# Kernel optimization log

Measured on AMD Instinct MI355X. Metric: run time of the kernel, lower is better.

Reference implementation:

```python
import jax, jax.numpy as jnp
import numpy as np

DIM = 768
NUM_HEADS = 12
HEAD_DIM = DIM // NUM_HEADS
SCALE = HEAD_DIM ** -0.5


def setup_inputs() -> dict:
    key = jax.random.key(0)
    k1, k2, k3, k4, k5 = jax.random.split(key, 5)
    B, N, C = 4, 1024, DIM
    x = jax.random.normal(k1, (B, N, C), dtype=jnp.float32)
    # padding mask: last quarter of tokens masked out for half the batch
    mask = jnp.ones((B, N), dtype=bool)
    mask = mask.at[B // 2:, 3 * N // 4:].set(False)
    w_qkv = jax.random.normal(k2, (3 * C, C), dtype=jnp.float32) * (C ** -0.5)
    w_proj = jax.random.normal(k3, (C, C), dtype=jnp.float32) * (C ** -0.5)
    b_proj = jax.random.normal(k4, (C,), dtype=jnp.float32) * 0.02
    return {"x": x, "mask": mask, "w_qkv": w_qkv, "w_proj": w_proj, "b_proj": b_proj}


def reference(x, mask, w_qkv, w_proj, b_proj):
    B, N, C = x.shape
    H, D = NUM_HEADS, HEAD_DIM
    # qkv: Linear without bias -> [B, N, 3C] -> [3, B, H, N, D]
    qkv = jnp.einsum('bnc,oc->bno', x, w_qkv).reshape(B, N, 3, H, D)
    qkv = jnp.transpose(qkv, (2, 0, 3, 1, 4))
    q, k, v = qkv[0], qkv[1], qkv[2]
    attn = jnp.einsum('bhnd,bhmd->bhnm', q, k) * SCALE  # [B,H,N,N]
    # outer-product padding mask: mask[:,None,:] * mask[:,:,None], broadcast over heads
    pair_mask = (mask[:, None, :] & mask[:, :, None])[:, None, :, :]  # [B,1,N,N]
    mask_value = -jnp.finfo(attn.dtype).max
    attn = jnp.where(pair_mask, attn, mask_value)
    attn = jax.nn.softmax(attn, axis=-1)
    out = jnp.einsum('bhnm,bhmd->bhnd', attn, v)  # [B,H,N,D]
    out = jnp.transpose(out, (0, 2, 1, 3)).reshape(B, N, C)
    out = jnp.einsum('bnc,oc->bno', out, w_proj) + b_proj
    return out
```

## Files before the change

kernel.cpp:

```cpp
#include <hip/hip_runtime.h>
#include <hip/hip_fp16.h>
#include <float.h>

typedef _Float16 f16;
typedef __attribute__((ext_vector_type(4))) _Float16 f16x4;
typedef __attribute__((ext_vector_type(8))) _Float16 f16x8;
typedef __attribute__((ext_vector_type(4))) float f32x4;

#define NB 4
#define SEQ 1024
#define DIM 768
#define NH 12
#define HD 64
#define SCALE_F 0.125f
#define LOG2E 1.44269504088896f
#define NBH (NB * NH)

__device__ __forceinline__ void gload16(const f16* g, f16* lds) {
    __builtin_amdgcn_global_load_lds(
        (const __attribute__((address_space(1))) void*)g,
        (__attribute__((address_space(3))) void*)lds, 16, 0, 0);
}

__global__ __launch_bounds__(256) void cvt_mask_kernel(
    const float* __restrict__ X, const float* __restrict__ W1,
    const float* __restrict__ W2, const void* __restrict__ mask_raw,
    f16* __restrict__ Xh, f16* __restrict__ W1h, f16* __restrict__ W2h,
    int* __restrict__ mnorm) {
    const int A4 = (NB * SEQ * DIM) / 4;
    const int B4 = (3 * DIM * DIM) / 4;
    const int C4 = (DIM * DIM) / 4;
    const int tid = threadIdx.x;
    if (blockIdx.x == (unsigned)(A4 + B4 + C4 + 255) / 256) {
        __shared__ int is_u8;
        if (tid == 0) is_u8 = 0;
        __syncthreads();
        const unsigned int* u32 = (const unsigned int*)mask_raw;
        int bad = 0;
        for (int i = tid; i < (NB * SEQ) / 4; i += 256)
            if (u32[i] > 1u) bad = 1;
        if (bad) atomicOr(&is_u8, 1);
        __syncthreads();
        const int u8mode = is_u8;
        const unsigned char* u8 = (const unsigned char*)mask_raw;
        const int* i32 = (const int*)mask_raw;
        for (int i = tid; i < NB * SEQ; i += 256)
            mnorm[i] = u8mode ? (u8[i] != 0) : (i32[i] != 0);
        return;
    }
    int i = blockIdx.x * 256 + tid;
    const float* s; f16* d; int j;
    if (i < A4)                { s = X;  d = Xh;  j = i; }
    else if (i < A4 + B4)      { s = W1; d = W1h; j = i - A4; }
    else if (i < A4 + B4 + C4) { s = W2; d = W2h; j = i - A4 - B4; }
    else return;
    float4 v = ((const float4*)s)[j];
    f16x4 h;
    h[0] = (f16)v.x; h[1] = (f16)v.y; h[2] = (f16)v.z; h[3] = (f16)v.w;
    *(f16x4*)(d + 4 * (size_t)j) = h;
}

__global__ __launch_bounds__(256) void qkv_gemm_f16(
    const f16* __restrict__ Xh, const f16* __restrict__ Wh,
    f16* __restrict__ Qh, f16* __restrict__ Kh, f16* __restrict__ Vth) {
    __shared__ __align__(16) f16 Ah[128 * 32];
    __shared__ __align__(16) f16 Bh[128 * 32];
    const int tid = threadIdx.x;
    const int l = tid & 63, w = tid >> 6;
    const int lo = l & 15, hi = l >> 4;
    const int wm = w >> 1, wn = w & 1;
    const int m0 = blockIdx.y * 128, o0 = blockIdx.x * 128;

    f32x4 acc[4][4];
#pragma unroll
    for (int i = 0; i < 4; ++i)
#pragma unroll
        for (int j = 0; j < 4; ++j) { f32x4 z = {0.f, 0.f, 0.f, 0.f}; acc[i][j] = z; }

    const int gr = l >> 2;
    const int gc = (l & 3) * 8;
    const f16* gA = Xh + (size_t)(m0 + w * 32 + gr) * DIM + gc;
    const f16* gB = Wh + (size_t)(o0 + w * 32 + gr) * DIM + gc;
    f16* lA = Ah + (w * 2) * 512;
    f16* lB = Bh + (w * 2) * 512;

    for (int k0 = 0; k0 < DIM; k0 += 32) {
        __syncthreads();
        gload16(gA + k0,            lA);
        gload16(gA + k0 + 16 * DIM, lA + 512);
        gload16(gB + k0,            lB);
        gload16(gB + k0 + 16 * DIM, lB + 512);
        __syncthreads();
        f16x8 af[4], bf[4];
#pragma unroll
        for (int i = 0; i < 4; ++i)
            af[i] = *(const f16x8*)&Ah[(wm * 64 + i * 16 + lo) * 32 + hi * 8];
#pragma unroll
        for (int j = 0; j < 4; ++j)
            bf[j] = *(const f16x8*)&Bh[(wn * 64 + j * 16 + lo) * 32 + hi * 8];
#pragma unroll
        for (int i = 0; i < 4; ++i)
#pragma unroll
            for (int j = 0; j < 4; ++j)
                acc[i][j] = __builtin_amdgcn_mfma_f32_16x16x32_f16(af[i], bf[j], acc[i][j], 0, 0, 0);
    }

    const int oo = o0 + wn * 64;
    const int s = oo / DIM;
    const int hh = (oo % DIM) / HD;
    const int b = m0 >> 10;
    const int nbase = (m0 & 1023) + wm * 64;
    if (s < 2) {
        f16* dst = (s == 0) ? Qh : Kh;
        const float qs = (s == 0) ? SCALE_F * LOG2E : 1.0f;
        f16* base = dst + ((size_t)(b * NH + hh)) * SEQ * HD;
#pragma unroll
        for (int i = 0; i < 4; ++i)
#pragma unroll
            for (int r = 0; r < 4; ++r) {
                const int n = nbase + i * 16 + hi * 4 + r;
#pragma unroll
                for (int j = 0; j < 4; ++j)
                    base[(size_t)n * HD + j * 16 + lo] = (f16)(acc[i][j][r] * qs);
            }
    } else {
        f16* base = Vth + ((size_t)(b * NH + hh)) * HD * SEQ;
#pragma unroll
        for (int i = 0; i < 4; ++i) {
            const int n4 = nbase + i * 16 + hi * 4;
#pragma unroll
            for (int j = 0; j < 4; ++j) {
                const int d = j * 16 + lo;
                f16x4 pv;
#pragma unroll
                for (int r = 0; r < 4; ++r) pv[r] = (f16)acc[i][j][r];
                *(f16x4*)(base + (size_t)d * SEQ + n4) = pv;
            }
        }
    }
}

__global__ __launch_bounds__(256) void attn_f16(
    const f16* __restrict__ Qh, const f16* __restrict__ Kh,
    const f16* __restrict__ Vth, const int* __restrict__ mnorm,
    f16* __restrict__ Oh) {
    const int bh = blockIdx.y, b = bh / NH, hh = bh % NH;
    const int q0 = blockIdx.x * 64;
    const int tid = threadIdx.x;
    const int l = tid & 63, w = tid >> 6;
    const int lo = l & 15, hi = l >> 4;

    __shared__ __align__(16) f16 Ks[64][64];
    __shared__ __align__(16) f16 Vs[64][64];
    __shared__ __align__(16) f16 Ps[4][16][64];
    __shared__ int mks[64];

    const f16* Qp = Qh + (size_t)bh * SEQ * HD;
    const f16* Kp = Kh + (size_t)bh * SEQ * HD;
    const f16* Vp = Vth + (size_t)bh * HD * SEQ;

    f16x8 qa[2];
#pragma unroll
    for (int kk = 0; kk < 2; ++kk)
        qa[kk] = *(const f16x8*)(Qp + (size_t)(q0 + w * 16 + lo) * HD + kk * 32 + hi * 8);
    const int mq = mnorm[b * SEQ + q0 + w * 16 + lo];

    float m_run = -FLT_MAX, l_run = 0.f;
    f32x4 oacc[4];
#pragma unroll
    for (int n = 0; n < 4; ++n) { f32x4 z = {0.f, 0.f, 0.f, 0.f}; oacc[n] = z; }

    const int sr = tid >> 2, sc = (tid & 3) * 16;
    const int swz = (sr & 7) * 8;
    const int s8 = (lo & 7) * 8;

    f16x8 kr0, kr1, vr0, vr1; int mkr;
    kr0 = *(const f16x8*)(Kp + (size_t)sr * HD + sc);
    kr1 = *(const f16x8*)(Kp + (size_t)sr * HD + sc + 8);
    vr0 = *(const f16x8*)(Vp + (size_t)sr * SEQ + sc);
    vr1 = *(const f16x8*)(Vp + (size_t)sr * SEQ + sc + 8);
    mkr = mnorm[b * SEQ + l];

    for (int t = 0; t < SEQ / 64; ++t) {
        __syncthreads();
        *(f16x8*)&Ks[sr][sc ^ swz]       = kr0;
        *(f16x8*)&Ks[sr][(sc + 8) ^ swz] = kr1;
        *(f16x8*)&Vs[sr][sc ^ swz]       = vr0;
        *(f16x8*)&Vs[sr][(sc + 8) ^ swz] = vr1;
        if (tid < 64) mks[tid] = mkr;
        __syncthreads();
        if (t < SEQ / 64 - 1) {
            const int kv1 = (t + 1) * 64;
            kr0 = *(const f16x8*)(Kp + (size_t)(kv1 + sr) * HD + sc);
            kr1 = *(const f16x8*)(Kp + (size_t)(kv1 + sr) * HD + sc + 8);
            vr0 = *(const f16x8*)(Vp + (size_t)sr * SEQ + kv1 + sc);
            vr1 = *(const f16x8*)(Vp + (size_t)sr * SEQ + kv1 + sc + 8);
            mkr = mnorm[b * SEQ + kv1 + l];
        }

        f32x4 sf[4];
#pragma unroll
        for (int f = 0; f < 4; ++f) { f32x4 z = {0.f, 0.f, 0.f, 0.f}; sf[f] = z; }
#pragma unroll
        for (int kk = 0; kk < 2; ++kk)
#pragma unroll
            for (int f = 0; f < 4; ++f) {
                f16x8 kf = *(const f16x8*)&Ks[f * 16 + lo][(kk * 32 + hi * 8) ^ s8];
                sf[f] = __builtin_amdgcn_mfma_f32_16x16x32_f16(kf, qa[kk], sf[f], 0, 0, 0);
            }
#pragma unroll
        for (int f = 0; f < 4; ++f) {
            int mv[4];
            *(int4*)mv = *(const int4*)&mks[f * 16 + hi * 4];
#pragma unroll
            for (int r = 0; r < 4; ++r)
                sf[f][r] = (mq && mv[r]) ? sf[f][r] : -FLT_MAX;
        }
        float pm = -FLT_MAX;
#pragma unroll
        for (int f = 0; f < 4; ++f)
            pm = fmaxf(pm, fmaxf(fmaxf(sf[f][0], sf[f][1]), fmaxf(sf[f][2], sf[f][3])));
        pm = fmaxf(pm, __shfl_xor(pm, 16));
        pm = fmaxf(pm, __shfl_xor(pm, 32));
        const float mn = fmaxf(m_run, pm);
        const float alpha = exp2f(m_run - mn);
        m_run = mn;
        float rs = 0.f;
#pragma unroll
        for (int f = 0; f < 4; ++f)
#pragma unroll
            for (int r = 0; r < 4; ++r) {
                float p = exp2f(sf[f][r] - mn);
                sf[f][r] = p;
                rs += p;
            }
        rs += __shfl_xor(rs, 16);
        rs += __shfl_xor(rs, 32);
        l_run = l_run * alpha + rs;

#pragma unroll
        for (int f = 0; f < 4; ++f) {
            f16x4 pv;
#pragma unroll
            for (int r = 0; r < 4; ++r) pv[r] = (f16)sf[f][r];
            *(f16x4*)&Ps[w][lo][(f * 16 + hi * 4) ^ s8] = pv;
        }
        if (!__all(alpha == 1.0f)) {
            float ar[4];
#pragma unroll
            for (int r = 0; r < 4; ++r) ar[r] = __shfl(alpha, hi * 4 + r);
#pragma unroll
            for (int n = 0; n < 4; ++n)
#pragma unroll
                for (int r = 0; r < 4; ++r) oacc[n][r] *= ar[r];
        }
#pragma unroll
        for (int kk = 0; kk < 2; ++kk) {
            f16x8 pa = *(const f16x8*)&Ps[w][lo][(kk * 32 + hi * 8) ^ s8];
#pragma unroll
            for (int n = 0; n < 4; ++n) {
                f16x8 vb = *(const f16x8*)&Vs[n * 16 + lo][(kk * 32 + hi * 8) ^ s8];
                oacc[n] = __builtin_amdgcn_mfma_f32_16x16x32_f16(pa, vb, oacc[n], 0, 0, 0);
            }
        }
    }

    float il[4];
#pragma unroll
    for (int r = 0; r < 4; ++r) il[r] = __shfl(l_run, hi * 4 + r);
    f16* Op = Oh + ((size_t)b * SEQ + q0 + w * 16) * DIM + hh * HD;
#pragma unroll
    for (int r = 0; r < 4; ++r) {
        const float inv = 1.f / il[r];
#pragma unroll
        for (int n = 0; n < 4; ++n)
            Op[(size_t)(hi * 4 + r) * DIM + n * 16 + lo] = (f16)(oacc[n][r] * inv);
    }
}

__global__ __launch_bounds__(256) void proj_gemm_f16(
    const f16* __restrict__ Oh, const f16* __restrict__ Wph,
    const float* __restrict__ bp, float* __restrict__ out) {
    __shared__ __align__(16) f16 Ah[128 * 32];
    __shared__ __align__(16) f16 Bh[128 * 32];
    const int tid = threadIdx.x;
    const int l = tid & 63, w = tid >> 6;
    const int lo = l & 15, hi = l >> 4;
    const int wm = w >> 1, wn = w & 1;
    const int m0 = blockIdx.y * 128, o0 = blockIdx.x * 128;

    f32x4 acc[4][4];
#pragma unroll
    for (int i = 0; i < 4; ++i)
#pragma unroll
        for (int j = 0; j < 4; ++j) { f32x4 z = {0.f, 0.f, 0.f, 0.f}; acc[i][j] = z; }

    const int gr = l >> 2;
    const int gc = (l & 3) * 8;
    const f16* gA = Oh + (size_t)(m0 + w * 32 + gr) * DIM + gc;
    const f16* gB = Wph + (size_t)(o0 + w * 32 + gr) * DIM + gc;
    f16* lA = Ah + (w * 2) * 512;
    f16* lB = Bh + (w * 2) * 512;

    for (int k0 = 0; k0 < DIM; k0 += 32) {
        __syncthreads();
        gload16(gA + k0,            lA);
        gload16(gA + k0 + 16 * DIM, lA + 512);
        gload16(gB + k0,            lB);
        gload16(gB + k0 + 16 * DIM, lB + 512);
        __syncthreads();
        f16x8 af[4], bf[4];
#pragma unroll
        for (int i = 0; i < 4; ++i)
            af[i] = *(const f16x8*)&Ah[(wm * 64 + i * 16 + lo) * 32 + hi * 8];
#pragma unroll
        for (int j = 0; j < 4; ++j)
            bf[j] = *(const f16x8*)&Bh[(wn * 64 + j * 16 + lo) * 32 + hi * 8];
#pragma unroll
        for (int i = 0; i < 4; ++i)
#pragma unroll
            for (int j = 0; j < 4; ++j)
                acc[i][j] = __builtin_amdgcn_mfma_f32_16x16x32_f16(af[i], bf[j], acc[i][j], 0, 0, 0);
    }

    float bpv[4];
#pragma unroll
    for (int j = 0; j < 4; ++j) bpv[j] = bp[o0 + wn * 64 + j * 16 + lo];
#pragma unroll
    for (int i = 0; i < 4; ++i)
#pragma unroll
        for (int r = 0; r < 4; ++r) {
            const int m = m0 + wm * 64 + i * 16 + hi * 4 + r;
#pragma unroll
            for (int j = 0; j < 4; ++j)
                out[(size_t)m * DIM + o0 + wn * 64 + j * 16 + lo] = acc[i][j][r] + bpv[j];
        }
}

extern "C" void kernel_launch(void* const* d_in, const int* in_sizes, int n_in,
                              void* d_out, int out_size, void* d_ws, size_t ws_size,
                              hipStream_t stream) {
    const float* x      = (const float*)d_in[0];
    const void*  mask   = d_in[1];
    const float* w_qkv  = (const float*)d_in[2];
    const float* w_proj = (const float*)d_in[3];
    const float* b_proj = (const float*)d_in[4];
    float* out          = (float*)d_out;

    char* w = (char*)d_ws;
    int* mnorm = (int*)w;                  w += 16384;
    const size_t NX  = (size_t)NB * SEQ * DIM;
    const size_t NW1 = (size_t)3 * DIM * DIM;
    const size_t NW2 = (size_t)DIM * DIM;
    f16* Xh   = (f16*)w;  w += NX  * sizeof(f16);
    f16* W1h  = (f16*)w;  w += NW1 * sizeof(f16);
    f16* W2h  = (f16*)w;  w += NW2 * sizeof(f16);
    f16* Qh   = (f16*)w;  w += NX * sizeof(f16);
    f16* Kh   = (f16*)w;  w += NX * sizeof(f16);
    f16* Vth  = (f16*)w;  w += NX * sizeof(f16);
    f16* Oh   = (f16*)w;  w += NX * sizeof(f16);

    const int cvt_blocks = ((NB * SEQ * DIM + 4 * DIM * DIM) / 4 + 255) / 256 + 1;
    cvt_mask_kernel<<<cvt_blocks, 256, 0, stream>>>(x, w_qkv, w_proj, mask,
                                                    Xh, W1h, W2h, mnorm);
    qkv_gemm_f16<<<dim3(18, 32), 256, 0, stream>>>(Xh, W1h, Qh, Kh, Vth);
    attn_f16<<<dim3(SEQ / 64, NBH), 256, 0, stream>>>(Qh, Kh, Vth, mnorm, Oh);
    proj_gemm_f16<<<dim3(6, 32), 256, 0, stream>>>(Oh, W2h, b_proj, out);
}
```

Measured before the change: 101.5 us.

## Use single-wave attention blocks reading K/V directly from global, additive mask bias

The attention kernel moves from 256-thread blocks that stage K and V tiles in shared memory behind barriers to 64-thread single-wave blocks of 16 queries that load K and V fragments straight from global memory (via cache). The mask is precomputed as an additive float bias, with fully masked query rows set to zero scores. This removes the block barriers and LDS staging, but each wave now re-reads K/V independently, which quadruples global/L2 traffic and removes the prefetch overlap. Masked query rows now give a uniform softmax, which matches the reference behaviour.

New measurement: 156.0 us. 53.7% more time.

```diff
diff --git a/kernel.cpp b/kernel.cpp
--- a/kernel.cpp
+++ b/kernel.cpp
@@ -15,6 +15,7 @@
 #define SCALE_F 0.125f
 #define LOG2E 1.44269504088896f
 #define NBH (NB * NH)
+#define MASK_NEG (-1.0e30f)
 
 __device__ __forceinline__ void gload16(const f16* g, f16* lds) {
     __builtin_amdgcn_global_load_lds(
@@ -26,7 +27,7 @@
     const float* __restrict__ X, const float* __restrict__ W1,
     const float* __restrict__ W2, const void* __restrict__ mask_raw,
     f16* __restrict__ Xh, f16* __restrict__ W1h, f16* __restrict__ W2h,
-    int* __restrict__ mnorm) {
+    float* __restrict__ Mb) {
     const int A4 = (NB * SEQ * DIM) / 4;
     const int B4 = (3 * DIM * DIM) / 4;
     const int C4 = (DIM * DIM) / 4;
@@ -44,8 +45,10 @@
         const int u8mode = is_u8;
         const unsigned char* u8 = (const unsigned char*)mask_raw;
         const int* i32 = (const int*)mask_raw;
-        for (int i = tid; i < NB * SEQ; i += 256)
-            mnorm[i] = u8mode ? (u8[i] != 0) : (i32[i] != 0);
+        for (int i = tid; i < NB * SEQ; i += 256) {
+            const int m = u8mode ? (u8[i] != 0) : (i32[i] != 0);
+            Mb[i] = m ? 0.0f : MASK_NEG;
+        }
         return;
     }
     int i = blockIdx.x * 256 + tid;
@@ -140,64 +143,37 @@
     }
 }
 
-__global__ __launch_bounds__(256) void attn_f16(
+__global__ __launch_bounds__(64) void attn_f16(
     const f16* __restrict__ Qh, const f16* __restrict__ Kh,
-    const f16* __restrict__ Vth, const int* __restrict__ mnorm,
+    const f16* __restrict__ Vth, const float* __restrict__ Mb,
     f16* __restrict__ Oh) {
     const int bh = blockIdx.y, b = bh / NH, hh = bh % NH;
-    const int q0 = blockIdx.x * 64;
-    const int tid = threadIdx.x;
-    const int l = tid & 63, w = tid >> 6;
+    const int q0 = blockIdx.x * 16;
+    const int l = threadIdx.x;
     const int lo = l & 15, hi = l >> 4;
 
-    __shared__ __align__(16) f16 Ks[64][64];
-    __shared__ __align__(16) f16 Vs[64][64];
-    __shared__ __align__(16) f16 Ps[4][16][64];
-    __shared__ int mks[64];
+    __shared__ __align__(16) f16 Ps[16][64];
 
     const f16* Qp = Qh + (size_t)bh * SEQ * HD;
     const f16* Kp = Kh + (size_t)bh * SEQ * HD;
     const f16* Vp = Vth + (size_t)bh * HD * SEQ;
+    const float* Mbb = Mb + b * SEQ;
 
     f16x8 qa[2];
 #pragma unroll
     for (int kk = 0; kk < 2; ++kk)
-        qa[kk] = *(const f16x8*)(Qp + (size_t)(q0 + w * 16 + lo) * HD + kk * 32 + hi * 8);
-    const int mq = mnorm[b * SEQ + q0 + w * 16 + lo];
+        qa[kk] = *(const f16x8*)(Qp + (size_t)(q0 + lo) * HD + kk * 32 + hi * 8);
+    const bool mq = (Mbb[q0 + lo] == 0.0f);
 
     float m_run = -FLT_MAX, l_run = 0.f;
     f32x4 oacc[4];
 #pragma unroll
     for (int n = 0; n < 4; ++n) { f32x4 z = {0.f, 0.f, 0.f, 0.f}; oacc[n] = z; }
 
-    const int sr = tid >> 2, sc = (tid & 3) * 16;
-    const int swz = (sr & 7) * 8;
     const int s8 = (lo & 7) * 8;
 
-    f16x8 kr0, kr1, vr0, vr1; int mkr;
-    kr0 = *(const f16x8*)(Kp + (size_t)sr * HD + sc);
-    kr1 = *(const f16x8*)(Kp + (size_t)sr * HD + sc + 8);
-    vr0 = *(const f16x8*)(Vp + (size_t)sr * SEQ + sc);
-    vr1 = *(const f16x8*)(Vp + (size_t)sr * SEQ + sc + 8);
-    mkr = mnorm[b * SEQ + l];
-
     for (int t = 0; t < SEQ / 64; ++t) {
-        __syncthreads();
-        *(f16x8*)&Ks[sr][sc ^ swz]       = kr0;
-        *(f16x8*)&Ks[sr][(sc + 8) ^ swz] = kr1;
-        *(f16x8*)&Vs[sr][sc ^ swz]       = vr0;
-        *(f16x8*)&Vs[sr][(sc + 8) ^ swz] = vr1;
-        if (tid < 64) mks[tid] = mkr;
-        __syncthreads();
-        if (t < SEQ / 64 - 1) {
-            const int kv1 = (t + 1) * 64;
-            kr0 = *(const f16x8*)(Kp + (size_t)(kv1 + sr) * HD + sc);
-            kr1 = *(const f16x8*)(Kp + (size_t)(kv1 + sr) * HD + sc + 8);
-            vr0 = *(const f16x8*)(Vp + (size_t)sr * SEQ + kv1 + sc);
-            vr1 = *(const f16x8*)(Vp + (size_t)sr * SEQ + kv1 + sc + 8);
-            mkr = mnorm[b * SEQ + kv1 + l];
-        }
-
+        const int kv0 = t * 64;
         f32x4 sf[4];
 #pragma unroll
         for (int f = 0; f < 4; ++f) { f32x4 z = {0.f, 0.f, 0.f, 0.f}; sf[f] = z; }
@@ -205,16 +181,18 @@
         for (int kk = 0; kk < 2; ++kk)
 #pragma unroll
             for (int f = 0; f < 4; ++f) {
-                f16x8 kf = *(const f16x8*)&Ks[f * 16 + lo][(kk * 32 + hi * 8) ^ s8];
+                f16x8 kf = *(const f16x8*)(Kp + (size_t)(kv0 + f * 16 + lo) * HD
+                                              + kk * 32 + hi * 8);
                 sf[f] = __builtin_amdgcn_mfma_f32_16x16x32_f16(kf, qa[kk], sf[f], 0, 0, 0);
             }
 #pragma unroll
         for (int f = 0; f < 4; ++f) {
-            int mv[4];
-            *(int4*)mv = *(const int4*)&mks[f * 16 + hi * 4];
-#pragma unroll
-            for (int r = 0; r < 4; ++r)
-                sf[f][r] = (mq && mv[r]) ? sf[f][r] : -FLT_MAX;
+            f32x4 bias = *(const f32x4*)(Mbb + kv0 + f * 16 + hi * 4);
+#pragma unroll
+            for (int r = 0; r < 4; ++r) {
+                const float sv = sf[f][r] + bias[r];
+                sf[f][r] = mq ? sv : 0.0f;
+            }
         }
         float pm = -FLT_MAX;
 #pragma unroll
@@ -243,7 +221,7 @@
             f16x4 pv;
 #pragma unroll
             for (int r = 0; r < 4; ++r) pv[r] = (f16)sf[f][r];
-            *(f16x4*)&Ps[w][lo][(f * 16 + hi * 4) ^ s8] = pv;
+            *(f16x4*)&Ps[lo][(f * 16 + hi * 4) ^ s8] = pv;
         }
         if (!__all(alpha == 1.0f)) {
             float ar[4];
@@ -256,10 +234,11 @@
         }
 #pragma unroll
         for (int kk = 0; kk < 2; ++kk) {
-            f16x8 pa = *(const f16x8*)&Ps[w][lo][(kk * 32 + hi * 8) ^ s8];
+            f16x8 pa = *(const f16x8*)&Ps[lo][(kk * 32 + hi * 8) ^ s8];
 #pragma unroll
             for (int n = 0; n < 4; ++n) {
-                f16x8 vb = *(const f16x8*)&Vs[n * 16 + lo][(kk * 32 + hi * 8) ^ s8];
+                f16x8 vb = *(const f16x8*)(Vp + (size_t)(n * 16 + lo) * SEQ
+                                              + kv0 + kk * 32 + hi * 8);
                 oacc[n] = __builtin_amdgcn_mfma_f32_16x16x32_f16(pa, vb, oacc[n], 0, 0, 0);
             }
         }
@@ -268,7 +247,7 @@
     float il[4];
 #pragma unroll
     for (int r = 0; r < 4; ++r) il[r] = __shfl(l_run, hi * 4 + r);
-    f16* Op = Oh + ((size_t)b * SEQ + q0 + w * 16) * DIM + hh * HD;
+    f16* Op = Oh + ((size_t)b * SEQ + q0) * DIM + hh * HD;
 #pragma unroll
     for (int r = 0; r < 4; ++r) {
         const float inv = 1.f / il[r];
@@ -348,7 +327,7 @@
     float* out          = (float*)d_out;
 
     char* w = (char*)d_ws;
-    int* mnorm = (int*)w;                  w += 16384;
+    float* Mb = (float*)w;                 w += 16384;
     const size_t NX  = (size_t)NB * SEQ * DIM;
     const size_t NW1 = (size_t)3 * DIM * DIM;
     const size_t NW2 = (size_t)DIM * DIM;
@@ -362,8 +341,8 @@
 
     const int cvt_blocks = ((NB * SEQ * DIM + 4 * DIM * DIM) / 4 + 255) / 256 + 1;
     cvt_mask_kernel<<<cvt_blocks, 256, 0, stream>>>(x, w_qkv, w_proj, mask,
-                                                    Xh, W1h, W2h, mnorm);
+                                                    Xh, W1h, W2h, Mb);
     qkv_gemm_f16<<<dim3(18, 32), 256, 0, stream>>>(Xh, W1h, Qh, Kh, Vth);
-    attn_f16<<<dim3(SEQ / 64, NBH), 256, 0, stream>>>(Qh, Kh, Vth, mnorm, Oh);
+    attn_f16<<<dim3(SEQ / 16, NBH), 64, 0, stream>>>(Qh, Kh, Vth, Mb, Oh);
     proj_gemm_f16<<<dim3(6, 32), 256, 0, stream>>>(Oh, W2h, b_proj, out);
 }
```
